# Optimization experiments

Measured on AMD Instinct MI355X. Metric: run time of the kernel, lower is better.

## Reference

```python
import jax, jax.numpy as jnp
import numpy as np
import math

NUM_HEADS = 32
NUM_KV_HEADS = 8
HEAD_DIM = 128
ROPE_THETA = 10000.0


def _rope_cos_sin(position_ids, head_dim, dtype):
    # inv_freq: [head_dim/2]
    inv_freq = 1.0 / (ROPE_THETA ** (jnp.arange(0, head_dim, 2, dtype=jnp.float32) / head_dim))
    # freqs: [B, S, head_dim/2]
    freqs = position_ids.astype(jnp.float32)[:, :, None] * inv_freq[None, None, :]
    emb = jnp.concatenate([freqs, freqs], axis=-1)  # [B, S, head_dim]
    return jnp.cos(emb).astype(dtype), jnp.sin(emb).astype(dtype)


def _rotate_half(x):
    h = x.shape[-1] // 2
    return jnp.concatenate([-x[..., h:], x[..., :h]], axis=-1)


def setup_inputs() -> dict:
    key = jax.random.key(0)
    ks = jax.random.split(key, 5)
    B, S, H = 1, 2048, 4096
    kv_dim = NUM_KV_HEADS * HEAD_DIM
    return {
        "hidden_states": jax.random.normal(ks[0], (B, S, H), dtype=jnp.float32),
        "position_ids": jnp.arange(S, dtype=jnp.int64 if jax.config.jax_enable_x64 else jnp.int32)[None, :].repeat(B, axis=0),
        "Wq": jax.random.normal(ks[1], (H, H), dtype=jnp.float32) * 0.02,
        "Wk": jax.random.normal(ks[2], (kv_dim, H), dtype=jnp.float32) * 0.02,
        "Wv": jax.random.normal(ks[3], (kv_dim, H), dtype=jnp.float32) * 0.02,
        "Wo": jax.random.normal(ks[4], (H, H), dtype=jnp.float32) * 0.02,
    }


def reference(hidden_states, position_ids, Wq, Wk, Wv, Wo):
    B, S, H = hidden_states.shape
    groups = NUM_HEADS // NUM_KV_HEADS

    # QKV projections (nn.Linear: x @ W.T, no bias)
    q = (hidden_states @ Wq.T).reshape(B, S, NUM_HEADS, HEAD_DIM).transpose(0, 2, 1, 3)
    k = (hidden_states @ Wk.T).reshape(B, S, NUM_KV_HEADS, HEAD_DIM).transpose(0, 2, 1, 3)
    v = (hidden_states @ Wv.T).reshape(B, S, NUM_KV_HEADS, HEAD_DIM).transpose(0, 2, 1, 3)

    # RoPE
    cos, sin = _rope_cos_sin(position_ids, HEAD_DIM, q.dtype)
    cos = cos[:, None, :, :]  # [B,1,S,hd]
    sin = sin[:, None, :, :]
    q = q * cos + _rotate_half(q) * sin
    k = k * cos + _rotate_half(k) * sin

    # repeat_kv: expand KV heads to match Q heads
    k = jnp.repeat(k, groups, axis=1)  # [B, NUM_HEADS, S, hd]
    v = jnp.repeat(v, groups, axis=1)

    # scores + causal mask + fp32 softmax
    scores = jnp.einsum("bhqd,bhkd->bhqk", q, k) / math.sqrt(HEAD_DIM)
    causal = jnp.tril(jnp.ones((S, S), dtype=bool))
    scores = jnp.where(causal[None, None, :, :], scores, jnp.finfo(jnp.float32).min)
    attn = jax.nn.softmax(scores.astype(jnp.float32), axis=-1).astype(q.dtype)

    # attention output + output projection
    out = jnp.einsum("bhqk,bhkd->bhqd", attn, v)
    out = out.transpose(0, 2, 1, 3).reshape(B, S, H)
    return out @ Wo.T
```

## Files before the change

### kernel.cpp

```cpp
#include <hip/hip_runtime.h>
#include <stdint.h>


typedef __attribute__((ext_vector_type(8))) __bf16 bf16x8;
typedef __attribute__((ext_vector_type(4))) float floatx4;

#define S_LEN 2048
#define HID   4096
#define NH    32
#define NKV   8
#define HD    128

__device__ __forceinline__ unsigned short f2bf(float f) {
  union { float f; uint32_t u; } v; v.f = f;
  return (unsigned short)((v.u + 0x7fffu + ((v.u >> 16) & 1u)) >> 16);
}

__device__ __forceinline__ void gload_lds16(const unsigned short* g, unsigned short* l) {
  __builtin_amdgcn_global_load_lds(
      (const __attribute__((address_space(1))) void*)g,
      (__attribute__((address_space(3))) void*)l,
      16, 0, 0);
}

__global__ void cast_bf16_kernel(const float* __restrict__ in,
                                 unsigned short* __restrict__ out, int n4) {
  int i = blockIdx.x * blockDim.x + threadIdx.x;
  if (i >= n4) return;
  float4 f = ((const float4*)in)[i];
  ushort4 o = make_ushort4(f2bf(f.x), f2bf(f.y), f2bf(f.z), f2bf(f.w));
  ((ushort4*)out)[i] = o;
}

#define GT 32

__global__ __launch_bounds__(512, 2) void gemm_bt256_kernel(
    const unsigned short* __restrict__ A,
    const unsigned short* __restrict__ B,
    float* __restrict__ C, int M, int N, int K) {
  __shared__ unsigned short As[4][256 * GT];
  __shared__ unsigned short Bs[4][256 * GT];
  const int m0 = blockIdx.y * 256;
  const int n0 = blockIdx.x * 256;
  const int tid = threadIdx.x;
  const int lane = tid & 63;
  const int wv = tid >> 6;
  const int wr = wv >> 2;
  const int wc = wv & 3;
  const int l15 = lane & 15;
  const int quad = lane >> 4;

  const int ch0 = wv * 64 + lane;
  const int ch1 = ch0 + 512;
  const int cs0 = ch0 ^ ((ch0 >> 3) & 3);
  const int cs1 = ch1 ^ ((ch1 >> 3) & 3);
  const int r0s = cs0 >> 2, c0s = (cs0 & 3) * 8;
  const int r1s = cs1 >> 2, c1s = (cs1 & 3) * 8;

  floatx4 acc[8][4];
#pragma unroll
  for (int i = 0; i < 8; i++)
#pragma unroll
    for (int j = 0; j < 4; j++) acc[i][j] = (floatx4){0.f, 0.f, 0.f, 0.f};

  const int T = K / GT;

#define STAGE_A(kk0, s)                                                        \
  do {                                                                         \
    gload_lds16(A + (size_t)(m0 + r0s) * K + (kk0) + c0s, &As[s][ch0 * 8]);    \
    gload_lds16(A + (size_t)(m0 + r1s) * K + (kk0) + c1s, &As[s][ch1 * 8]);    \
  } while (0)
#define STAGE_B(kk0, s)                                                        \
  do {                                                                         \
    gload_lds16(B + (size_t)(n0 + r0s) * K + (kk0) + c0s, &Bs[s][ch0 * 8]);    \
    gload_lds16(B + (size_t)(n0 + r1s) * K + (kk0) + c1s, &Bs[s][ch1 * 8]);    \
  } while (0)

  STAGE_A(0, 0);  STAGE_B(0, 0);
  STAGE_A(GT, 1); STAGE_B(GT, 1);
  STAGE_A(2 * GT, 2); STAGE_B(2 * GT, 2);
  asm volatile("s_waitcnt vmcnt(8)" ::: "memory");
  __builtin_amdgcn_s_barrier();

  for (int t = 0; t < T; ++t) {
    const int s = t & 3;
    const int sn = (t + 3) & 3;
    const bool pf = (t + 3 < T);
    const int kpf = (t + 3) * GT;

    bf16x8 bfr[4], afr[4];
#pragma unroll
    for (int ni = 0; ni < 4; ++ni) {
      const int row = wc * 64 + ni * 16 + l15;
      bfr[ni] = *(const bf16x8*)&Bs[s][row * GT + (((quad ^ (row >> 1)) & 3) * 8)];
    }
#pragma unroll
    for (int mi = 0; mi < 4; ++mi) {
      const int row = wr * 128 + mi * 16 + l15;
      afr[mi] = *(const bf16x8*)&As[s][row * GT + (((quad ^ (row >> 1)) & 3) * 8)];
    }
    if (pf) STAGE_A(kpf, sn);
    __builtin_amdgcn_s_barrier();
    asm volatile("s_waitcnt lgkmcnt(0)" ::: "memory");
    __builtin_amdgcn_sched_barrier(0);
    __builtin_amdgcn_s_setprio(1);
#pragma unroll
    for (int mi = 0; mi < 4; ++mi)
#pragma unroll
      for (int ni = 0; ni < 4; ++ni)
        acc[mi][ni] = __builtin_amdgcn_mfma_f32_16x16x32_bf16(
            afr[mi], bfr[ni], acc[mi][ni], 0, 0, 0);
    __builtin_amdgcn_s_setprio(0);
    __builtin_amdgcn_sched_barrier(0);
    __builtin_amdgcn_s_barrier();

#pragma unroll
    for (int mi = 0; mi < 4; ++mi) {
      const int row = wr * 128 + (mi + 4) * 16 + l15;
      afr[mi] = *(const bf16x8*)&As[s][row * GT + (((quad ^ (row >> 1)) & 3) * 8)];
    }
    if (pf) STAGE_B(kpf, sn);
    __builtin_amdgcn_s_barrier();
    asm volatile("s_waitcnt lgkmcnt(0)" ::: "memory");
    __builtin_amdgcn_sched_barrier(0);
    __builtin_amdgcn_s_setprio(1);
#pragma unroll
    for (int mi = 0; mi < 4; ++mi)
#pragma unroll
      for (int ni = 0; ni < 4; ++ni)
        acc[mi + 4][ni] = __builtin_amdgcn_mfma_f32_16x16x32_bf16(
            afr[mi], bfr[ni], acc[mi + 4][ni], 0, 0, 0);
    __builtin_amdgcn_s_setprio(0);
    __builtin_amdgcn_sched_barrier(0);
    if (t + 3 < T)      { asm volatile("s_waitcnt vmcnt(8)" ::: "memory"); }
    else if (t + 2 < T) { asm volatile("s_waitcnt vmcnt(4)" ::: "memory"); }
    else if (t + 1 < T) { asm volatile("s_waitcnt vmcnt(0)" ::: "memory"); }
    __builtin_amdgcn_s_barrier();
  }
#undef STAGE_A
#undef STAGE_B

#pragma unroll
  for (int mi = 0; mi < 8; ++mi) {
    const int row = m0 + wr * 128 + mi * 16 + quad * 4;
#pragma unroll
    for (int ni = 0; ni < 4; ++ni) {
      const int col = n0 + wc * 64 + ni * 16 + l15;
#pragma unroll
      for (int r = 0; r < 4; ++r)
        C[(size_t)(row + r) * N + col] = acc[mi][ni][r];
    }
  }
}

#define BM 128
#define BN 128
#define BK 32

__global__ __launch_bounds__(256) void gemm_bt_kernel(
    const unsigned short* __restrict__ A,
    const unsigned short* __restrict__ B,
    float* __restrict__ C, int M, int N, int K) {
  __shared__ unsigned short As[BM * BK];
  __shared__ unsigned short Bs[BN * BK];
  const int m0 = blockIdx.y * BM;
  const int n0 = blockIdx.x * BN;
  const int tid = threadIdx.x;
  const int lane = tid & 63;
  const int l15 = lane & 15;
  const int quad = lane >> 4;
  const int w = tid >> 6;
  const int wm = (w >> 1) * 64;
  const int wn = (w & 1) * 64;

  floatx4 acc[4][4];
#pragma unroll
  for (int i = 0; i < 4; i++)
#pragma unroll
    for (int j = 0; j < 4; j++) acc[i][j] = (floatx4){0.f, 0.f, 0.f, 0.f};

  const int c0 = tid, c1 = tid + 256;
  const int r0 = c0 >> 2, o0 = (c0 & 3) * 8;
  const int r1 = c1 >> 2, o1 = (c1 & 3) * 8;

  for (int k0 = 0; k0 < K; k0 += BK) {
    __syncthreads();
    gload_lds16(A + (size_t)(m0 + r0) * K + k0 + o0, As + c0 * 8);
    gload_lds16(A + (size_t)(m0 + r1) * K + k0 + o1, As + c1 * 8);
    gload_lds16(B + (size_t)(n0 + r0) * K + k0 + o0, Bs + c0 * 8);
    gload_lds16(B + (size_t)(n0 + r1) * K + k0 + o1, Bs + c1 * 8);
    __syncthreads();

    bf16x8 a_frag[4], b_frag[4];
#pragma unroll
    for (int mt = 0; mt < 4; mt++)
      a_frag[mt] = *(const bf16x8*)&As[(wm + mt * 16 + l15) * BK + quad * 8];
#pragma unroll
    for (int nt = 0; nt < 4; nt++)
      b_frag[nt] = *(const bf16x8*)&Bs[(wn + nt * 16 + l15) * BK + quad * 8];
#pragma unroll
    for (int mt = 0; mt < 4; mt++)
#pragma unroll
      for (int nt = 0; nt < 4; nt++)
        acc[mt][nt] = __builtin_amdgcn_mfma_f32_16x16x32_bf16(
            a_frag[mt], b_frag[nt], acc[mt][nt], 0, 0, 0);
  }

#pragma unroll
  for (int mt = 0; mt < 4; mt++) {
#pragma unroll
    for (int nt = 0; nt < 4; nt++) {
      const int row = m0 + wm + mt * 16 + quad * 4;
      const int col = n0 + wn + nt * 16 + l15;
#pragma unroll
      for (int r = 0; r < 4; r++)
        C[(size_t)(row + r) * N + col] = acc[mt][nt][r];
    }
  }
}

__global__ void rope_kernel(const float* __restrict__ Cqkv,
                            const int* __restrict__ pos_ids,
                            unsigned short* __restrict__ Qb,
                            unsigned short* __restrict__ Kb) {
  int t = blockIdx.x * blockDim.x + threadIdx.x;
  int j = t & 63;
  int s = t >> 6;
  int hh = blockIdx.y;
  float pos = (float)pos_ids[s];
  float ang = pos * exp2f(-0.20762050593045222f * (float)j);
  float c = cosf(ang), sn = sinf(ang);
  if (hh < NH) {
    const float* row = Cqkv + (size_t)s * 6144 + hh * HD;
    float x1 = row[j], x2 = row[j + 64];
    unsigned short* q = Qb + ((size_t)hh * S_LEN + s) * HD;
    q[j]      = f2bf(x1 * c - x2 * sn);
    q[j + 64] = f2bf(x2 * c + x1 * sn);
  } else {
    int kh = hh - NH;
    const float* row = Cqkv + (size_t)s * 6144 + HID + kh * HD;
    float x1 = row[j], x2 = row[j + 64];
    unsigned short* k = Kb + ((size_t)kh * S_LEN + s) * HD;
    k[j]      = f2bf(x1 * c - x2 * sn);
    k[j + 64] = f2bf(x2 * c + x1 * sn);
  }
}

__global__ void vtrans_kernel(const float* __restrict__ Cqkv,
                              unsigned short* __restrict__ Vt) {
  int t = blockIdx.x * blockDim.x + threadIdx.x;
  int s = t & (S_LEN - 1);
  int d = (t >> 11) & (HD - 1);
  int kh = t >> 18;
  Vt[((size_t)kh * HD + d) * S_LEN + s] =
      f2bf(Cqkv[(size_t)s * 6144 + (HID + NKV * HD) + kh * HD + d]);
}

__global__ __launch_bounds__(256, 2) void flash_attn_kernel(
    const unsigned short* __restrict__ Qb, const unsigned short* __restrict__ Kb,
    const unsigned short* __restrict__ Vt, unsigned short* __restrict__ O) {
  __shared__ unsigned short Ks[2][64 * 128];
  __shared__ unsigned short Vs[2][128 * 64];
  __shared__ unsigned short Ps[4][2][16 * 64];
  const int qb = gridDim.x - 1 - blockIdx.x;
  const int q0 = qb * 128;
  const int h = blockIdx.y;
  const int kvh = h >> 2;
  const int tid = threadIdx.x;
  const int lane = tid & 63;
  const int w = tid >> 6;
  const int l15 = lane & 15;
  const int quad = lane >> 4;
  const int qlo = q0 + w * 32;

  const unsigned short* Qh = Qb + (size_t)h * S_LEN * HD;
  const unsigned short* Kh = Kb + (size_t)kvh * S_LEN * HD;
  const unsigned short* Vh = Vt + (size_t)kvh * HD * S_LEN;

  const int nkt = q0 / 64 + 2;

#pragma unroll
  for (int it = 0; it < 4; it++) {
    int c = tid + it * 256;
    int kr = c >> 4, kj = (c & 15) ^ (kr & 15);
    gload_lds16(Kh + (size_t)kr * HD + kj * 8, Ks[0] + c * 8);
    int vd = c >> 3, vj = (c & 7) ^ (vd & 7);
    gload_lds16(Vh + (size_t)vd * S_LEN + vj * 8, Vs[0] + c * 8);
  }

  bf16x8 q_frag[2][4];
#pragma unroll
  for (int mf = 0; mf < 2; mf++)
#pragma unroll
    for (int kk = 0; kk < 4; kk++)
      q_frag[mf][kk] = *(const bf16x8*)&Qh[(size_t)(qlo + mf * 16 + l15) * HD + kk * 32 + quad * 8];

  bf16x8 ones_frag;
  {
    union { unsigned short u; __bf16 b; } ov;
    ov.u = (l15 == 0) ? 0x3F80 : 0;
#pragma unroll
    for (int j = 0; j < 8; j++) ones_frag[j] = ov.b;
  }

  floatx4 o_acc[2][8];
  floatx4 o_l[2];
#pragma unroll
  for (int mf = 0; mf < 2; mf++) {
#pragma unroll
    for (int i = 0; i < 8; i++) o_acc[mf][i] = (floatx4){0.f, 0.f, 0.f, 0.f};
    o_l[mf] = (floatx4){0.f, 0.f, 0.f, 0.f};
  }
  const float SC2 = 0.12751738f;

  for (int kt = 0; kt < nkt; kt++) {
    const int kbase = kt * 64;
    const int buf = kt & 1;
    __syncthreads();

    if (kt + 1 < nkt) {
      const int kb2 = kbase + 64;
#pragma unroll
      for (int it = 0; it < 4; it++) {
        int c = tid + it * 256;
        int kr = c >> 4, kj = (c & 15) ^ (kr & 15);
        gload_lds16(Kh + (size_t)(kb2 + kr) * HD + kj * 8, Ks[buf ^ 1] + c * 8);
        int vd = c >> 3, vj = (c & 7) ^ (vd & 7);
        gload_lds16(Vh + (size_t)vd * S_LEN + kb2 + vj * 8, Vs[buf ^ 1] + c * 8);
      }
    }

    if (kbase <= qlo + 31) {
      floatx4 s_acc[2][4];
#pragma unroll
      for (int mf = 0; mf < 2; mf++)
#pragma unroll
        for (int nt = 0; nt < 4; nt++) s_acc[mf][nt] = (floatx4){0.f, 0.f, 0.f, 0.f};
#pragma unroll
      for (int kk = 0; kk < 4; kk++)
#pragma unroll
        for (int nt = 0; nt < 4; nt++) {
          bf16x8 k_frag = *(const bf16x8*)&Ks[buf][(nt * 16 + l15) * 128 + (((kk * 4 + quad) ^ l15) * 8)];
#pragma unroll
          for (int mf = 0; mf < 2; mf++)
            s_acc[mf][nt] = __builtin_amdgcn_mfma_f32_16x16x32_bf16(
                q_frag[mf][kk], k_frag, s_acc[mf][nt], 0, 0, 0);
        }

      const bool diag = (kbase + 63 > qlo);
#pragma unroll
      for (int mf = 0; mf < 2; mf++) {
#pragma unroll
        for (int nt = 0; nt < 4; nt++) {
          int kc = kbase + nt * 16 + l15;
          int qrow = qlo + mf * 16 + quad * 4;
          int chunk2 = nt * 2 + (l15 >> 3);
          int coff = l15 & 7;
#pragma unroll
          for (int r = 0; r < 4; r++) {
            float pv = exp2f(s_acc[mf][nt][r] * SC2);
            if (diag && kc > qrow + r) pv = 0.f;
            int row = quad * 4 + r;
            Ps[w][mf][row * 64 + ((chunk2 ^ (row & 7)) * 8) + coff] = f2bf(pv);
          }
        }
      }

#pragma unroll
      for (int kk2 = 0; kk2 < 2; kk2++) {
        bf16x8 p_frag[2];
#pragma unroll
        for (int mf = 0; mf < 2; mf++)
          p_frag[mf] = *(const bf16x8*)&Ps[w][mf][l15 * 64 + (((kk2 * 4 + quad) ^ (l15 & 7)) * 8)];
#pragma unroll
        for (int dt = 0; dt < 8; dt++) {
          bf16x8 v_frag = *(const bf16x8*)&Vs[buf][(dt * 16 + l15) * 64 + (((kk2 * 4 + quad) ^ (l15 & 7)) * 8)];
#pragma unroll
          for (int mf = 0; mf < 2; mf++)
            o_acc[mf][dt] = __builtin_amdgcn_mfma_f32_16x16x32_bf16(
                p_frag[mf], v_frag, o_acc[mf][dt], 0, 0, 0);
        }
#pragma unroll
        for (int mf = 0; mf < 2; mf++)
          o_l[mf] = __builtin_amdgcn_mfma_f32_16x16x32_bf16(
              p_frag[mf], ones_frag, o_l[mf], 0, 0, 0);
      }
    }
  }

#pragma unroll
  for (int mf = 0; mf < 2; mf++)
#pragma unroll
    for (int r = 0; r < 4; r++) {
      float lsum = __shfl(o_l[mf][r], lane & 48, 64);
      float inv = 1.f / lsum;
      int qr = qlo + mf * 16 + quad * 4 + r;
#pragma unroll
      for (int dt = 0; dt < 8; dt++)
        O[(size_t)qr * HID + h * HD + dt * 16 + l15] = f2bf(o_acc[mf][dt][r] * inv);
    }
}

extern "C" void kernel_launch(void* const* d_in, const int* in_sizes, int n_in,
                              void* d_out, int out_size, void* d_ws, size_t ws_size,
                              hipStream_t stream) {
  const float* hidden = (const float*)d_in[0];
  const int*   pos    = (const int*)d_in[1];
  const float* Wq     = (const float*)d_in[2];
  const float* Wk     = (const float*)d_in[3];
  const float* Wv     = (const float*)d_in[4];
  const float* Wo     = (const float*)d_in[5];

  char* ws = (char*)d_ws;
  size_t off = 0;
  unsigned short* h_b    = (unsigned short*)(ws + off); off += (size_t)S_LEN * HID * 2;
  unsigned short* Wqkv_b = (unsigned short*)(ws + off); off += (size_t)6144 * HID * 2;
  unsigned short* Wo_b   = (unsigned short*)(ws + off); off += (size_t)HID * HID * 2;
  float*          Cqkv   = (float*)(ws + off);          off += (size_t)S_LEN * 6144 * 4;
  unsigned short* Qb     = (unsigned short*)(ws + off); off += (size_t)NH * S_LEN * HD * 2;
  unsigned short* Kb     = (unsigned short*)(ws + off); off += (size_t)NKV * S_LEN * HD * 2;
  unsigned short* Vt     = (unsigned short*)(ws + off); off += (size_t)NKV * HD * S_LEN * 2;
  unsigned short* attn_b = (unsigned short*)Cqkv;

  cast_bf16_kernel<<<(S_LEN * HID / 4) / 256, 256, 0, stream>>>(hidden, h_b, S_LEN * HID / 4);
  cast_bf16_kernel<<<(HID * HID / 4) / 256, 256, 0, stream>>>(Wq, Wqkv_b, HID * HID / 4);
  cast_bf16_kernel<<<(1024 * HID / 4) / 256, 256, 0, stream>>>(Wk, Wqkv_b + (size_t)4096 * HID, 1024 * HID / 4);
  cast_bf16_kernel<<<(1024 * HID / 4) / 256, 256, 0, stream>>>(Wv, Wqkv_b + (size_t)5120 * HID, 1024 * HID / 4);
  cast_bf16_kernel<<<(HID * HID / 4) / 256, 256, 0, stream>>>(Wo, Wo_b, HID * HID / 4);

  gemm_bt256_kernel<<<dim3(6144 / 256, S_LEN / 256), 512, 0, stream>>>(h_b, Wqkv_b, Cqkv, S_LEN, 6144, HID);

  rope_kernel<<<dim3(S_LEN * 64 / 256, NH + NKV), 256, 0, stream>>>(Cqkv, pos, Qb, Kb);
  vtrans_kernel<<<(NKV * HD * S_LEN) / 256, 256, 0, stream>>>(Cqkv, Vt);

  flash_attn_kernel<<<dim3(S_LEN / 128, NH), 256, 0, stream>>>(Qb, Kb, Vt, attn_b);

  gemm_bt_kernel<<<dim3(HID / BN, S_LEN / BM), 256, 0, stream>>>(attn_b, Wo_b, (float*)d_out, S_LEN, HID, HID);
}
```

Before: 589.2 us.

## Double-buffer GEMM fragments in registers with one barrier per k-step

Restructures the bf16 GEMM main loop to load all A and B fragments for the next k-tile from LDS into a second register set while the MFMA burst runs on the current set. The A and B global-to-LDS prefetches are merged into a single stage issue, and the loop drops from several barriers per k-step to one. The aim is to hide LDS read latency behind MFMA work and cut synchronisation overhead. In exchange it holds 24 fragment registers alongside 128 accumulator floats under a 512-thread, 2-block launch bound, which risks register spills or lower occupancy.

```diff
diff --git a/kernel.cpp b/kernel.cpp
--- a/kernel.cpp
+++ b/kernel.cpp
@@ -33,6 +33,30 @@
 }
 
 #define GT 32
+
+__device__ __forceinline__ void read_frags12(
+    bf16x8* f, const unsigned short* AsS, const unsigned short* BsS,
+    int wr, int wc, int l15, int quad) {
+#pragma unroll
+  for (int mi = 0; mi < 8; ++mi) {
+    const int row = wr * 128 + mi * 16 + l15;
+    f[mi] = *(const bf16x8*)&AsS[row * GT + (((quad ^ (row >> 1)) & 3) * 8)];
+  }
+#pragma unroll
+  for (int ni = 0; ni < 4; ++ni) {
+    const int row = wc * 64 + ni * 16 + l15;
+    f[8 + ni] = *(const bf16x8*)&BsS[row * GT + (((quad ^ (row >> 1)) & 3) * 8)];
+  }
+}
+
+__device__ __forceinline__ void mfma_burst32(const bf16x8* f, floatx4 (*acc)[4]) {
+#pragma unroll
+  for (int mi = 0; mi < 8; ++mi)
+#pragma unroll
+    for (int ni = 0; ni < 4; ++ni)
+      acc[mi][ni] = __builtin_amdgcn_mfma_f32_16x16x32_bf16(
+          f[mi], f[8 + ni], acc[mi][ni], 0, 0, 0);
+}
 
 __global__ __launch_bounds__(512, 2) void gemm_bt256_kernel(
     const unsigned short* __restrict__ A,
@@ -65,80 +89,50 @@
 
   const int T = K / GT;
 
-#define STAGE_A(kk0, s)                                                        \
+#define STAGE_T(kk0, s)                                                        \
   do {                                                                         \
     gload_lds16(A + (size_t)(m0 + r0s) * K + (kk0) + c0s, &As[s][ch0 * 8]);    \
     gload_lds16(A + (size_t)(m0 + r1s) * K + (kk0) + c1s, &As[s][ch1 * 8]);    \
-  } while (0)
-#define STAGE_B(kk0, s)                                                        \
-  do {                                                                         \
     gload_lds16(B + (size_t)(n0 + r0s) * K + (kk0) + c0s, &Bs[s][ch0 * 8]);    \
     gload_lds16(B + (size_t)(n0 + r1s) * K + (kk0) + c1s, &Bs[s][ch1 * 8]);    \
   } while (0)
 
-  STAGE_A(0, 0);  STAGE_B(0, 0);
-  STAGE_A(GT, 1); STAGE_B(GT, 1);
-  STAGE_A(2 * GT, 2); STAGE_B(2 * GT, 2);
-  asm volatile("s_waitcnt vmcnt(8)" ::: "memory");
+  STAGE_T(0, 0);
+  STAGE_T(GT, 1);
+  STAGE_T(2 * GT, 2);
+  asm volatile("s_waitcnt vmcnt(4)" ::: "memory");
   __builtin_amdgcn_s_barrier();
 
-  for (int t = 0; t < T; ++t) {
-    const int s = t & 3;
-    const int sn = (t + 3) & 3;
-    const bool pf = (t + 3 < T);
-    const int kpf = (t + 3) * GT;
-
-    bf16x8 bfr[4], afr[4];
-#pragma unroll
-    for (int ni = 0; ni < 4; ++ni) {
-      const int row = wc * 64 + ni * 16 + l15;
-      bfr[ni] = *(const bf16x8*)&Bs[s][row * GT + (((quad ^ (row >> 1)) & 3) * 8)];
-    }
-#pragma unroll
-    for (int mi = 0; mi < 4; ++mi) {
-      const int row = wr * 128 + mi * 16 + l15;
-      afr[mi] = *(const bf16x8*)&As[s][row * GT + (((quad ^ (row >> 1)) & 3) * 8)];
-    }
-    if (pf) STAGE_A(kpf, sn);
-    __builtin_amdgcn_s_barrier();
-    asm volatile("s_waitcnt lgkmcnt(0)" ::: "memory");
-    __builtin_amdgcn_sched_barrier(0);
-    __builtin_amdgcn_s_setprio(1);
-#pragma unroll
-    for (int mi = 0; mi < 4; ++mi)
-#pragma unroll
-      for (int ni = 0; ni < 4; ++ni)
-        acc[mi][ni] = __builtin_amdgcn_mfma_f32_16x16x32_bf16(
-            afr[mi], bfr[ni], acc[mi][ni], 0, 0, 0);
-    __builtin_amdgcn_s_setprio(0);
-    __builtin_amdgcn_sched_barrier(0);
-    __builtin_amdgcn_s_barrier();
-
-#pragma unroll
-    for (int mi = 0; mi < 4; ++mi) {
-      const int row = wr * 128 + (mi + 4) * 16 + l15;
-      afr[mi] = *(const bf16x8*)&As[s][row * GT + (((quad ^ (row >> 1)) & 3) * 8)];
-    }
-    if (pf) STAGE_B(kpf, sn);
-    __builtin_amdgcn_s_barrier();
-    asm volatile("s_waitcnt lgkmcnt(0)" ::: "memory");
-    __builtin_amdgcn_sched_barrier(0);
-    __builtin_amdgcn_s_setprio(1);
-#pragma unroll
-    for (int mi = 0; mi < 4; ++mi)
-#pragma unroll
-      for (int ni = 0; ni < 4; ++ni)
-        acc[mi + 4][ni] = __builtin_amdgcn_mfma_f32_16x16x32_bf16(
-            afr[mi], bfr[ni], acc[mi + 4][ni], 0, 0, 0);
-    __builtin_amdgcn_s_setprio(0);
-    __builtin_amdgcn_sched_barrier(0);
-    if (t + 3 < T)      { asm volatile("s_waitcnt vmcnt(8)" ::: "memory"); }
-    else if (t + 2 < T) { asm volatile("s_waitcnt vmcnt(4)" ::: "memory"); }
-    else if (t + 1 < T) { asm volatile("s_waitcnt vmcnt(0)" ::: "memory"); }
-    __builtin_amdgcn_s_barrier();
-  }
-#undef STAGE_A
-#undef STAGE_B
+  bf16x8 fA[12], fB[12];
+  read_frags12(fA, As[0], Bs[0], wr, wc, l15, quad);
+  asm volatile("s_waitcnt lgkmcnt(0)" ::: "memory");
+  __builtin_amdgcn_sched_barrier(0);
+
+#define BODY(tt, CUR, NXT)                                                     \
+  do {                                                                         \
+    const int t_ = (tt);                                                       \
+    if (t_ + 1 < T)                                                            \
+      read_frags12(NXT, As[(t_ + 1) & 3], Bs[(t_ + 1) & 3], wr, wc, l15, quad);\
+    if (t_ + 3 < T) STAGE_T((t_ + 3) * GT, (t_ + 3) & 3);                      \
+    __builtin_amdgcn_sched_barrier(0);                                         \
+    __builtin_amdgcn_s_setprio(1);                                             \
+    mfma_burst32(CUR, acc);                                                    \
+    __builtin_amdgcn_s_setprio(0);                                             \
+    __builtin_amdgcn_sched_barrier(0);                                         \
+    asm volatile("s_waitcnt lgkmcnt(0)" ::: "memory");                         \
+                  \
+    if (t_ + 3 < T)      { asm volatile("s_waitcnt vmcnt(4)" ::: "memory"); }  \
+    else if (t_ + 2 < T) { asm volatile("s_waitcnt vmcnt(0)" ::: "memory"); }  \
+    __builtin_amdgcn_sched_barrier(0);                                         \
+    __builtin_amdgcn_s_barrier();                                              \
+  } while (0)
+
+  for (int t = 0; t < T; t += 2) {
+    BODY(t, fA, fB);
+    BODY(t + 1, fB, fA);
+  }
+#undef BODY
+#undef STAGE_T
 
 #pragma unroll
   for (int mi = 0; mi < 8; ++mi) {
```

Result: no change. 578.9 us (-1.8%).
